# Kernel tuning notes

Hardware: AMD Instinct MI355X
Metric: run time of the kernel (lower is better)

Reference implementation:

```python
import jax, jax.numpy as jnp
import numpy as np

QP = 127.0          # signed symmetric 8-bit: Qp = 2**(8-1)-1
MIN_RANGE = 1e-6


def _ste_round(q):
    # round_pass: straight-through estimator round
    return q + jax.lax.stop_gradient(jnp.round(q) - q)


def _quant_per_token(x):
    # symmetric per-token: amax over last dim, keepdim
    s = jnp.clip(jnp.max(jnp.abs(x), axis=-1, keepdims=True), MIN_RANGE, None) / QP
    return _ste_round(x / s), s


def _quant_per_tensor(w):
    s = jnp.clip(jnp.max(jnp.abs(w)), MIN_RANGE, None) / QP
    return _ste_round(w / s), s


def _qlinear(x2d, w, b):
    # fake-quant linear: quantize act per-token, weight per-tensor,
    # int-domain matmul, bias added before dequant rescale (faithful to source)
    qx, sx = _quant_per_token(x2d)      # [N,K], [N,1]
    qw, sw = _quant_per_tensor(w)       # [M,K], scalar
    out = jnp.matmul(qx, qw.T) + b[None, :]
    return out * (sx * sw)              # [N,M]


def setup_inputs() -> dict:
    key = jax.random.key(0)
    k1, k2, k3, k4, k5 = jax.random.split(key, 5)
    B, S, D, H = 64, 197, 768, 3072
    return {
        "x": jax.random.normal(k1, (B, S, D), dtype=jnp.float32),
        "w1": jax.random.normal(k2, (H, D), dtype=jnp.float32) * 0.02,
        "b1": jax.random.normal(k3, (H,), dtype=jnp.float32) * 0.02,
        "w2": jax.random.normal(k4, (D, H), dtype=jnp.float32) * 0.02,
        "b2": jax.random.normal(k5, (D,), dtype=jnp.float32) * 0.02,
    }


def reference(x, w1, b1, w2, b2):
    B, S, D = x.shape
    x2d = x.reshape(-1, D)                         # view(-1, x.size(-1))
    h = _qlinear(x2d, w1, b1)                      # fc1
    h = jax.nn.gelu(h, approximate=False)          # ViT Mlp activation (exact GELU)
    o = _qlinear(h, w2, b2)                        # fc2
    return o.reshape(B, S, -1)
```

## Files before the change

### kernel.cpp

```cpp
#include <hip/hip_runtime.h>
#include <stdint.h>

#define QPF  127.0f
#define MINR 1e-6f

typedef int v4i __attribute__((ext_vector_type(4)));
typedef float f4v __attribute__((ext_vector_type(4)));
typedef _Float16 h4v __attribute__((ext_vector_type(4)));
typedef _Float16 h8 __attribute__((ext_vector_type(8)));
typedef signed char c8 __attribute__((ext_vector_type(8)));

__device__ __forceinline__ float wave_max64(float v) {
  v = fmaxf(v, __shfl_xor(v, 32, 64));
  v = fmaxf(v, __shfl_xor(v, 16, 64));
  v = fmaxf(v, __shfl_xor(v, 8, 64));
  v = fmaxf(v, __shfl_xor(v, 4, 64));
  v = fmaxf(v, __shfl_xor(v, 2, 64));
  v = fmaxf(v, __shfl_xor(v, 1, 64));
  return v;
}

__device__ __forceinline__ float gelu_exact(float x) {
  float z = fabsf(x) * 0.70710678118654752440f;
  float t = __builtin_amdgcn_rcpf(fmaf(0.3275911f, z, 1.0f));
  float p = fmaf(fmaf(fmaf(fmaf(1.061405429f, t, -1.453152027f), t,
                           1.421413741f), t, -0.284496736f), t, 0.254829592f) * t;
  float e = __expf(-z * z);
  float erfz = fmaf(-p, e, 1.0f);
  float cdf = fmaf(0.5f, copysignf(erfz, x), 0.5f);
  return x * cdf;
}

__device__ __forceinline__ void gl2lds16(const void* g, void* l) {
  __builtin_amdgcn_global_load_lds(
      (const __attribute__((address_space(1))) int*)g,
      (__attribute__((address_space(3))) int*)l,
      16, 0, 0);
}

__device__ __forceinline__ int xcd_swizzle(int flat, int nwg) {
  const int xcd = flat & 7;
  const int idx = flat >> 3;
  const int q = nwg >> 3, r = nwg & 7;
  const int base = (xcd < r) ? xcd * (q + 1) : r * (q + 1) + (xcd - r) * q;
  return base + idx;
}

__global__ __launch_bounds__(256) void pre_kernel(
    const float* __restrict__ w1, const float* __restrict__ w2, int n4,
    const float* __restrict__ x, signed char* __restrict__ qx,
    float* __restrict__ sx, unsigned* __restrict__ amaxh,
    float* __restrict__ partial, int K, int nTok) {
  __shared__ float red[4];
  const int b = blockIdx.x;
  const int tid = threadIdx.x;
  const int lane = tid & 63, wvi = tid >> 6;

  if (b < 1024) {
    const float4* w4 = (const float4*)(b < 512 ? w1 : w2);
    const int bb = b & 511;
    float m = 0.f;
    for (int i = bb * 256 + tid; i < n4; i += 512 * 256) {
      float4 v = w4[i];
      m = fmaxf(m, fmaxf(fmaxf(fabsf(v.x), fabsf(v.y)),
                         fmaxf(fabsf(v.z), fabsf(v.w))));
    }
    m = wave_max64(m);
    if (lane == 0) red[wvi] = m;
    __syncthreads();
    if (tid == 0)
      partial[b] = fmaxf(fmaxf(red[0], red[1]), fmaxf(red[2], red[3]));
  } else {
    const int token = (b - 1024) * 4 + wvi;
    if (token < nTok) {
      const int k4 = K >> 2;
      const float4* xr = (const float4*)(x + (size_t)token * K);
      float m = 0.f;
      for (int i = lane; i < k4; i += 64) {
        float4 v = xr[i];
        m = fmaxf(m, fmaxf(fmaxf(fabsf(v.x), fabsf(v.y)),
                           fmaxf(fabsf(v.z), fabsf(v.w))));
      }
      m = wave_max64(m);
      const float s = fmaxf(m, MINR) / QPF;
      const float rs = 1.0f / s;
      if (lane == 0) { sx[token] = s; amaxh[token] = 0u; }
      char4* q4 = (char4*)(qx + (size_t)token * K);
      for (int i = lane; i < k4; i += 64) {
        float4 v = xr[i];
        char4 c;
        c.x = (signed char)(int)rintf(v.x * rs);
        c.y = (signed char)(int)rintf(v.y * rs);
        c.z = (signed char)(int)rintf(v.z * rs);
        c.w = (signed char)(int)rintf(v.w * rs);
        q4[i] = c;
      }
    }
  }
}

__global__ __launch_bounds__(256) void wquant2_kernel(
    const float* __restrict__ w1, const float* __restrict__ w2, int n4,
    const float* __restrict__ partial, unsigned* __restrict__ wamax,
    signed char* __restrict__ q1, signed char* __restrict__ q2) {
  __shared__ float red[4];
  const int tid = threadIdx.x;
  const int lane = tid & 63, wvi = tid >> 6;
  const int y = blockIdx.y;
  float m = fmaxf(partial[y * 512 + tid], partial[y * 512 + 256 + tid]);
  m = wave_max64(m);
  if (lane == 0) red[wvi] = m;
  __syncthreads();
  const float M = fmaxf(fmaxf(red[0], red[1]), fmaxf(red[2], red[3]));
  if (blockIdx.x == 0 && tid == 0) wamax[y] = __float_as_uint(M);
  const float s = fmaxf(M, MINR) / QPF;
  const float rs = 1.0f / s;
  const float4* w4 = (const float4*)(y ? w2 : w1);
  char4* q4 = (char4*)(y ? q2 : q1);
  for (int i = blockIdx.x * 256 + tid; i < n4; i += gridDim.x * 256) {
    float4 v = w4[i];
    char4 c;
    c.x = (signed char)(int)rintf(v.x * rs);
    c.y = (signed char)(int)rintf(v.y * rs);
    c.z = (signed char)(int)rintf(v.z * rs);
    c.w = (signed char)(int)rintf(v.w * rs);
    q4[i] = c;
  }
}

__global__ __launch_bounds__(256) void hquant4_kernel(
    const _Float16* __restrict__ h, const unsigned* __restrict__ amaxbits,
    signed char* __restrict__ qh, float* __restrict__ sh, int K) {
  const int token = blockIdx.x * 4 + (threadIdx.x >> 6);
  const int lane = threadIdx.x & 63;
  const float s = fmaxf(__uint_as_float(amaxbits[token]), MINR) / QPF;
  const float rs = 1.0f / s;
  if (lane == 0) sh[token] = s;
  const h8* hr = (const h8*)(h + (size_t)token * K);
  c8* qr = (c8*)(qh + (size_t)token * K);
  for (int i = lane; i < (K >> 3); i += 64) {
    h8 v = hr[i];
    c8 c;
#pragma unroll
    for (int j = 0; j < 8; j++)
      c[j] = (signed char)(int)rintf((float)v[j] * rs);
    qr[i] = c;
  }
}

__global__ __launch_bounds__(256, 2) void gemm1_i8(
    const signed char* __restrict__ A, const signed char* __restrict__ B,
    const float* __restrict__ bias, const float* __restrict__ sA,
    const unsigned* __restrict__ sBbits, _Float16* __restrict__ out,
    unsigned* __restrict__ amax_out, int N, int K, int Mout) {
  __shared__ __align__(16) signed char lds[3 * 16384];

  const int t = threadIdx.x;
  const int lane = t & 63;
  const int wv = t >> 6;
  const int wm = wv >> 1;
  const int wn = wv & 1;

  const int nwg = gridDim.x * gridDim.y;
  const int wg = xcd_swizzle(blockIdx.x + gridDim.x * blockIdx.y, nwg);
  const int colBlk = (wg % gridDim.x) * 128;
  const int rowBlk = (wg / gridDim.x) * 128;

  int ar0 = rowBlk + wv * 16 + (lane >> 2);
  int ar1 = ar0 + 64;
  if (ar0 > N - 1) ar0 = N - 1;
  if (ar1 > N - 1) ar1 = N - 1;
  const int br0 = colBlk + wv * 16 + (lane >> 2);
  const int br1 = br0 + 64;
  const int kb = (((lane & 3) ^ ((lane >> 3) & 3)) * 16);

  const signed char* gA0 = A + (size_t)ar0 * K + kb;
  const signed char* gA1 = A + (size_t)ar1 * K + kb;
  const signed char* gB0 = B + (size_t)br0 * K + kb;
  const signed char* gB1 = B + (size_t)br1 * K + kb;

  const v4i vzero = {0, 0, 0, 0};
  v4i acc[4][4];
#pragma unroll
  for (int i = 0; i < 4; i++)
#pragma unroll
    for (int j = 0; j < 4; j++) acc[i][j] = vzero;

  const int swz = ((lane >> 4) ^ ((lane >> 1) & 3)) * 16;
  const int aoff = (wm * 64 + (lane & 15)) * 64 + swz;
  const int boff = (wn * 64 + (lane & 15)) * 64 + swz + 8192;

  const int T = K >> 6;

  auto issue = [&](int bufo) {
    signed char* a = lds + bufo + wv * 1024;
    gl2lds16(gA0, a);
    gl2lds16(gA1, a + 4096);
    gl2lds16(gB0, a + 8192);
    gl2lds16(gB1, a + 12288);
    gA0 += 64; gA1 += 64; gB0 += 64; gB1 += 64;
  };

  issue(0);
  issue(16384);

  int cur = 0;
  for (int kt = 0; kt < T; ++kt) {
    asm volatile("" ::: "memory");
    if (kt < T - 1)
      __builtin_amdgcn_s_waitcnt(0x0074);
    else
      __builtin_amdgcn_s_waitcnt(0x0070);
    __builtin_amdgcn_s_barrier();
    asm volatile("" ::: "memory");

    if (kt + 2 < T) {
      int pf = cur + 32768;
      if (pf >= 49152) pf -= 49152;
      issue(pf);
    }

    v4i a[4], b[4];
#pragma unroll
    for (int mi = 0; mi < 4; mi++)
      a[mi] = *(const v4i*)(lds + cur + aoff + mi * 1024);
#pragma unroll
    for (int ni = 0; ni < 4; ni++)
      b[ni] = *(const v4i*)(lds + cur + boff + ni * 1024);
#pragma unroll
    for (int mi = 0; mi < 4; mi++)
#pragma unroll
      for (int ni = 0; ni < 4; ni++)
        acc[mi][ni] = __builtin_amdgcn_mfma_i32_16x16x64_i8(b[ni], a[mi],
                                                            acc[mi][ni], 0, 0, 0);
    cur += 16384;
    if (cur >= 49152) cur = 0;
  }

  const float sB = fmaxf(__uint_as_float(*sBbits), MINR) / QPF;
  const int col0 = colBlk + wn * 64 + (lane >> 4) * 4;

  f4v bv[4];
#pragma unroll
  for (int ni = 0; ni < 4; ni++) bv[ni] = *(const f4v*)(bias + col0 + ni * 16);

#pragma unroll
  for (int mi = 0; mi < 4; mi++) {
    const int grow = rowBlk + wm * 64 + mi * 16 + (lane & 15);
    const float ss = ((grow < N) ? sA[grow] : 0.f) * sB;
    float rmax = 0.f;
#pragma unroll
    for (int ni = 0; ni < 4; ni++) {
      h4v hv;
#pragma unroll
      for (int r = 0; r < 4; r++) {
        float v = ((float)acc[mi][ni][r] + bv[ni][r]) * ss;
        v = gelu_exact(v);
        rmax = fmaxf(rmax, fabsf(v));
        hv[r] = (_Float16)v;
      }
      if (grow < N)
        *(h4v*)(out + (size_t)grow * Mout + col0 + ni * 16) = hv;
    }
    rmax = fmaxf(rmax, __shfl_xor(rmax, 16, 64));
    rmax = fmaxf(rmax, __shfl_xor(rmax, 32, 64));
    if (lane < 16 && grow < N)
      atomicMax(amax_out + grow, __float_as_uint(rmax));
  }
}

__global__ __launch_bounds__(256, 2) void gemm2_i8(
    const signed char* __restrict__ A, const signed char* __restrict__ B,
    const float* __restrict__ bias, const float* __restrict__ sA,
    const unsigned* __restrict__ sBbits, float* __restrict__ out,
    int N, int K, int Mout) {
  __shared__ __align__(16) signed char lds[3 * 16384];

  const int t = threadIdx.x;
  const int lane = t & 63;
  const int wv = t >> 6;
  const int wm = wv >> 1;
  const int wn = wv & 1;

  const int nwg = gridDim.x * gridDim.y;
  const int wg = xcd_swizzle(blockIdx.x + gridDim.x * blockIdx.y, nwg);
  const int colBlk = (wg % gridDim.x) * 128;
  const int rowBlk = (wg / gridDim.x) * 128;

  int ar0 = rowBlk + wv * 16 + (lane >> 2);
  int ar1 = ar0 + 64;
  if (ar0 > N - 1) ar0 = N - 1;
  if (ar1 > N - 1) ar1 = N - 1;
  const int br0 = colBlk + wv * 16 + (lane >> 2);
  const int br1 = br0 + 64;
  const int kb = (((lane & 3) ^ ((lane >> 3) & 3)) * 16);

  const signed char* gA0 = A + (size_t)ar0 * K + kb;
  const signed char* gA1 = A + (size_t)ar1 * K + kb;
  const signed char* gB0 = B + (size_t)br0 * K + kb;
  const signed char* gB1 = B + (size_t)br1 * K + kb;

  const v4i vzero = {0, 0, 0, 0};
  v4i acc[4][4];
#pragma unroll
  for (int i = 0; i < 4; i++)
#pragma unroll
    for (int j = 0; j < 4; j++) acc[i][j] = vzero;

  const int swz = ((lane >> 4) ^ ((lane >> 1) & 3)) * 16;
  const int aoff = (wm * 64 + (lane & 15)) * 64 + swz;
  const int boff = (wn * 64 + (lane & 15)) * 64 + swz + 8192;

  const int T = K >> 6;

  auto issue = [&](int bufo) {
    signed char* a = lds + bufo + wv * 1024;
    gl2lds16(gA0, a);
    gl2lds16(gA1, a + 4096);
    gl2lds16(gB0, a + 8192);
    gl2lds16(gB1, a + 12288);
    gA0 += 64; gA1 += 64; gB0 += 64; gB1 += 64;
  };

  issue(0);
  issue(16384);

  int cur = 0;
  for (int kt = 0; kt < T; ++kt) {
    asm volatile("" ::: "memory");
    if (kt < T - 1)
      __builtin_amdgcn_s_waitcnt(0x0074);
    else
      __builtin_amdgcn_s_waitcnt(0x0070);
    __builtin_amdgcn_s_barrier();
    asm volatile("" ::: "memory");

    if (kt + 2 < T) {
      int pf = cur + 32768;
      if (pf >= 49152) pf -= 49152;
      issue(pf);
    }

    v4i a[4], b[4];
#pragma unroll
    for (int mi = 0; mi < 4; mi++)
      a[mi] = *(const v4i*)(lds + cur + aoff + mi * 1024);
#pragma unroll
    for (int ni = 0; ni < 4; ni++)
      b[ni] = *(const v4i*)(lds + cur + boff + ni * 1024);
#pragma unroll
    for (int mi = 0; mi < 4; mi++)
#pragma unroll
      for (int ni = 0; ni < 4; ni++)
        acc[mi][ni] = __builtin_amdgcn_mfma_i32_16x16x64_i8(b[ni], a[mi],
                                                            acc[mi][ni], 0, 0, 0);
    cur += 16384;
    if (cur >= 49152) cur = 0;
  }

  const float sB = fmaxf(__uint_as_float(*sBbits), MINR) / QPF;
  const int col0 = colBlk + wn * 64 + (lane >> 4) * 4;

  f4v bv[4];
#pragma unroll
  for (int ni = 0; ni < 4; ni++) bv[ni] = *(const f4v*)(bias + col0 + ni * 16);

#pragma unroll
  for (int mi = 0; mi < 4; mi++) {
    const int grow = rowBlk + wm * 64 + mi * 16 + (lane & 15);
    const float ss = ((grow < N) ? sA[grow] : 0.f) * sB;
#pragma unroll
    for (int ni = 0; ni < 4; ni++) {
      f4v o;
#pragma unroll
      for (int r = 0; r < 4; r++)
        o[r] = ((float)acc[mi][ni][r] + bv[ni][r]) * ss;
      if (grow < N)
        *(f4v*)(out + (size_t)grow * Mout + col0 + ni * 16) = o;
    }
  }
}

extern "C" void kernel_launch(void* const* d_in, const int* in_sizes, int n_in,
                              void* d_out, int out_size, void* d_ws, size_t ws_size,
                              hipStream_t stream) {
  const float* x  = (const float*)d_in[0];
  const float* w1 = (const float*)d_in[1];
  const float* b1 = (const float*)d_in[2];
  const float* w2 = (const float*)d_in[3];
  const float* b2 = (const float*)d_in[4];

  const int H = in_sizes[2];
  const int D = in_sizes[4];
  const int N = in_sizes[0] / D;
  float* out = (float*)d_out;

  char* ws = (char*)d_ws;
  auto alloc = [&](size_t bytes) {
    char* p = ws;
    ws += (bytes + 255) & ~(size_t)255;
    return p;
  };
  signed char* qx  = (signed char*)alloc((size_t)N * D);
  signed char* qw1 = (signed char*)alloc((size_t)H * D);
  signed char* qw2 = (signed char*)alloc((size_t)H * D);
  signed char* qh  = (signed char*)alloc((size_t)N * H);
  float*    sx     = (float*)alloc((size_t)N * 4);
  float*    sh     = (float*)alloc((size_t)N * 4);
  unsigned* amaxh  = (unsigned*)alloc((size_t)N * 4);
  unsigned* wamax  = (unsigned*)alloc(256);
  float*    partial= (float*)alloc(1024 * 4);
  _Float16* h      = (_Float16*)alloc((size_t)N * H * 2);
  (void)ws_size;

  const int n4w = (H * D) >> 2;

  pre_kernel<<<1024 + (N + 3) / 4, 256, 0, stream>>>(w1, w2, n4w, x, qx, sx,
                                                     amaxh, partial, D, N);
  wquant2_kernel<<<dim3(512, 2), 256, 0, stream>>>(w1, w2, n4w, partial, wamax,
                                                   qw1, qw2);

  dim3 g1(H / 128, (N + 127) / 128);
  gemm1_i8<<<g1, 256, 0, stream>>>(qx, qw1, b1, sx, wamax + 0, h, amaxh,
                                   N, D, H);
  hquant4_kernel<<<N / 4, 256, 0, stream>>>(h, amaxh, qh, sh, H);

  dim3 g2(D / 128, (N + 127) / 128);
  gemm2_i8<<<g2, 256, 0, stream>>>(qh, qw2, b2, sh, wamax + 1, out, N, H, D);
}
```

Measured before the change: 234.3 us.

## Enlarge gemm1 workgroup tile to 256x128 with eight waves

```diff
diff --git a/kernel.cpp b/kernel.cpp
--- a/kernel.cpp
+++ b/kernel.cpp
@@ -148,12 +148,12 @@
   }
 }
 
-__global__ __launch_bounds__(256, 2) void gemm1_i8(
+__global__ __launch_bounds__(512, 4) void gemm1_i8(
     const signed char* __restrict__ A, const signed char* __restrict__ B,
     const float* __restrict__ bias, const float* __restrict__ sA,
     const unsigned* __restrict__ sBbits, _Float16* __restrict__ out,
     unsigned* __restrict__ amax_out, int N, int K, int Mout) {
-  __shared__ __align__(16) signed char lds[3 * 16384];
+  __shared__ __align__(16) signed char lds[3 * 24576];
 
   const int t = threadIdx.x;
   const int lane = t & 63;
@@ -164,20 +164,27 @@
   const int nwg = gridDim.x * gridDim.y;
   const int wg = xcd_swizzle(blockIdx.x + gridDim.x * blockIdx.y, nwg);
   const int colBlk = (wg % gridDim.x) * 128;
-  const int rowBlk = (wg / gridDim.x) * 128;
-
-  int ar0 = rowBlk + wv * 16 + (lane >> 2);
-  int ar1 = ar0 + 64;
-  if (ar0 > N - 1) ar0 = N - 1;
-  if (ar1 > N - 1) ar1 = N - 1;
-  const int br0 = colBlk + wv * 16 + (lane >> 2);
-  const int br1 = br0 + 64;
+  const int rowBlk = (wg / gridDim.x) * 256;
+
   const int kb = (((lane & 3) ^ ((lane >> 3) & 3)) * 16);
-
-  const signed char* gA0 = A + (size_t)ar0 * K + kb;
-  const signed char* gA1 = A + (size_t)ar1 * K + kb;
-  const signed char* gB0 = B + (size_t)br0 * K + kb;
-  const signed char* gB1 = B + (size_t)br1 * K + kb;
+  const int rr = lane >> 2;
+
+  const signed char* gp[3];
+  int ldo[3];
+#pragma unroll
+  for (int j = 0; j < 3; j++) {
+    const int c = wv + 8 * j;
+    if (c < 16) {
+      int r = rowBlk + c * 16 + rr;
+      if (r > N - 1) r = N - 1;
+      gp[j] = A + (size_t)r * K + kb;
+      ldo[j] = c * 1024;
+    } else {
+      const int r = colBlk + (c - 16) * 16 + rr;
+      gp[j] = B + (size_t)r * K + kb;
+      ldo[j] = 16384 + (c - 16) * 1024;
+    }
+  }
 
   const v4i vzero = {0, 0, 0, 0};
   v4i acc[4][4];
@@ -188,35 +195,34 @@
 
   const int swz = ((lane >> 4) ^ ((lane >> 1) & 3)) * 16;
   const int aoff = (wm * 64 + (lane & 15)) * 64 + swz;
-  const int boff = (wn * 64 + (lane & 15)) * 64 + swz + 8192;
+  const int boff = 16384 + (wn * 64 + (lane & 15)) * 64 + swz;
 
   const int T = K >> 6;
 
   auto issue = [&](int bufo) {
-    signed char* a = lds + bufo + wv * 1024;
-    gl2lds16(gA0, a);
-    gl2lds16(gA1, a + 4096);
-    gl2lds16(gB0, a + 8192);
-    gl2lds16(gB1, a + 12288);
-    gA0 += 64; gA1 += 64; gB0 += 64; gB1 += 64;
+#pragma unroll
+    for (int j = 0; j < 3; j++) {
+      gl2lds16(gp[j], lds + bufo + ldo[j]);
+      gp[j] += 64;
+    }
   };
 
   issue(0);
-  issue(16384);
+  issue(24576);
 
   int cur = 0;
   for (int kt = 0; kt < T; ++kt) {
     asm volatile("" ::: "memory");
     if (kt < T - 1)
-      __builtin_amdgcn_s_waitcnt(0x0074);
+      __builtin_amdgcn_s_waitcnt(0x0073);
     else
       __builtin_amdgcn_s_waitcnt(0x0070);
     __builtin_amdgcn_s_barrier();
     asm volatile("" ::: "memory");
 
     if (kt + 2 < T) {
-      int pf = cur + 32768;
-      if (pf >= 49152) pf -= 49152;
+      int pf = cur + 49152;
+      if (pf >= 73728) pf -= 73728;
       issue(pf);
     }
 
@@ -233,8 +239,8 @@
       for (int ni = 0; ni < 4; ni++)
         acc[mi][ni] = __builtin_amdgcn_mfma_i32_16x16x64_i8(b[ni], a[mi],
                                                             acc[mi][ni], 0, 0, 0);
-    cur += 16384;
-    if (cur >= 49152) cur = 0;
+    cur += 24576;
+    if (cur >= 73728) cur = 0;
   }
 
   const float sB = fmaxf(__uint_as_float(*sBbits), MINR) / QPF;
@@ -420,8 +426,8 @@
   wquant2_kernel<<<dim3(512, 2), 256, 0, stream>>>(w1, w2, n4w, partial, wamax,
                                                    qw1, qw2);
 
-  dim3 g1(H / 128, (N + 127) / 128);
-  gemm1_i8<<<g1, 256, 0, stream>>>(qx, qw1, b1, sx, wamax + 0, h, amaxh,
+  dim3 g1(H / 128, (N + 255) / 256);
+  gemm1_i8<<<g1, 512, 0, stream>>>(qx, qw1, b1, sx, wamax + 0, h, amaxh,
                                    N, D, H);
   hquant4_kernel<<<N / 4, 256, 0, stream>>>(h, amaxh, qh, sh, H);
 
```

Result: no change. 233.5 us (-0.4%).
